# Optimization experiments

Hardware: AMD Instinct MI355X
Metric: run time of the kernel (lower is better)

The kernel has to match this reference:

```python
import jax, jax.numpy as jnp
import numpy as np

P = 128        # num proposals
C_ALL = 19     # instance_classes + 1
C = 18         # instance classes used in the loop
M = 400000     # total (proposal, point) membership entries
N_PTS = 65536  # num points
SCORE_THR = 0.001
MASK_THR = -0.5
NPOINT_THR = 100


def setup_inputs() -> dict:
    key = jax.random.key(0)
    k1, k2, k3, k4, k5 = jax.random.split(key, 5)
    return {
        "cls_scores": jax.random.normal(k1, (P, C_ALL), dtype=jnp.float32),
        "scores": jax.random.normal(k2, (P, C_ALL), dtype=jnp.float32),
        "mask_scores": jax.random.normal(k3, (M, C_ALL), dtype=jnp.float32),
        "prop_ids": jax.random.randint(k4, (M,), 0, P, dtype=jnp.int32),
        "point_ids": jax.random.randint(k5, (M,), 0, N_PTS, dtype=jnp.int32),
        "num_points": N_PTS,
    }


def reference(cls_scores, scores, mask_scores, prop_ids, point_ids, num_points):
    # cls_scores, scores: [P, C+1]; mask_scores: [M, C+1]
    # prop_ids/point_ids: [M] -> membership of point in proposal
    n_prop = cls_scores.shape[0]
    cls_soft = jax.nn.softmax(cls_scores, axis=1)              # [P, C+1]
    # scores_pred_i = clamp(scores[:, i], 0, 1) * cls_soft[:, i], for each class i
    scores_pred = (jnp.clip(scores[:, :C], 0.0, 1.0) * cls_soft[:, :C]).T  # [C, P]

    # per-class mask threshold then scatter 1s into dense [P, N] proposal masks
    mask_keep = (mask_scores[:, :C] > MASK_THR).astype(jnp.int32).T        # [C, M]

    def scatter_one_class(m):
        # duplicates resolved with max (matches repeated assignment of 1)
        return jnp.zeros((n_prop, num_points), jnp.int32).at[prop_ids, point_ids].max(m)

    dense = jax.vmap(scatter_one_class)(mask_keep)             # [C, P, N] int32

    pointnum = dense.sum(axis=-1)                              # [C, P]
    keep = (cls_soft[:, :C].T > SCORE_THR) \
        & (scores_pred > -1.0) \
        & (pointnum >= NPOINT_THR)                             # [C, P]

    proposals_pred = dense * keep[..., None].astype(jnp.int32)  # zero invalid rows
    cluster_scores = jnp.where(keep, scores_pred, 0.0)
    semantic_id = jnp.broadcast_to((jnp.arange(C) + 1)[:, None], (C, n_prop))
    return proposals_pred, cluster_scores, keep, semantic_id
```

## Files before the change

kernel.cpp:

```cpp
#include <hip/hip_runtime.h>
#include <stdint.h>

#define NPROP   128
#define C_ALL   19
#define NCLS    18
#define M_TOTAL 400000
#define NPTS    65536
#define CP      (NCLS * NPROP)
#define PTS_PER_CHUNK 8192
#define NCHUNK  8

typedef float f32x4 __attribute__((ext_vector_type(4)));

struct WS {
    float        spred[CP];
    unsigned int keepA[CP];
    unsigned int pointnum[CP];
    unsigned int dense[(size_t)NPROP * NPTS];
};

__global__ void zero_prep_kernel(const float* __restrict__ cls_scores,
                                 const float* __restrict__ scores, WS* ws) {
    const size_t tid = (size_t)blockIdx.x * blockDim.x + threadIdx.x;
    const size_t stride = (size_t)gridDim.x * blockDim.x;
    uint4* d4 = (uint4*)ws->dense;
    const size_t n4 = (size_t)NPROP * NPTS / 4;
    const uint4 z = make_uint4(0u, 0u, 0u, 0u);
    for (size_t j = tid; j < n4; j += stride) d4[j] = z;
    if (tid < CP) ws->pointnum[tid] = 0;
    if (tid < NPROP) {
        const int p = (int)tid;
        float row[C_ALL];
        float mx = -3.4e38f;
        #pragma unroll
        for (int i = 0; i < C_ALL; ++i) {
            row[i] = cls_scores[p * C_ALL + i];
            mx = fmaxf(mx, row[i]);
        }
        float s = 0.0f;
        #pragma unroll
        for (int i = 0; i < C_ALL; ++i) {
            row[i] = __expf(row[i] - mx);
            s += row[i];
        }
        const float inv = 1.0f / s;
        #pragma unroll
        for (int c = 0; c < NCLS; ++c) {
            const float soft = row[c] * inv;
            float sc = scores[p * C_ALL + c];
            sc = fminf(fmaxf(sc, 0.0f), 1.0f);
            const float sp = sc * soft;
            ws->spred[c * NPROP + p] = sp;
            ws->keepA[c * NPROP + p] = (soft > 0.001f && sp > -1.0f) ? 1u : 0u;
        }
    }
}

__global__ void scatter_kernel(const float* __restrict__ mask_scores,
                               const int* __restrict__ prop_ids,
                               const int* __restrict__ point_ids,
                               WS* ws) {
    int m = blockIdx.x * blockDim.x + threadIdx.x;
    if (m >= M_TOTAL) return;
    const float* r = mask_scores + (size_t)m * C_ALL;
    unsigned int bits = 0;
    #pragma unroll
    for (int c = 0; c < NCLS; ++c)
        bits |= (unsigned int)(r[c] > -0.5f) << c;
    const size_t addr = ((size_t)prop_ids[m] << 16) | (unsigned int)point_ids[m];
    atomicOr(&ws->dense[addr], bits);
}

__global__ __launch_bounds__(256) void count_kernel(WS* ws) {
    __shared__ unsigned int cnt[NCLS];
    const int p = blockIdx.x;
    const int quarter = blockIdx.y;
    const int t = threadIdx.x;
    if (t < NCLS) cnt[t] = 0;
    __syncthreads();
    const uint4* base4 = (const uint4*)(ws->dense + ((size_t)p << 16) +
                                        quarter * (NPTS / 4));
    unsigned int local[NCLS];
    #pragma unroll
    for (int c = 0; c < NCLS; ++c) local[c] = 0;
    #pragma unroll
    for (int j = 0; j < (NPTS / 16) / 256; ++j) {
        const uint4 w = base4[j * 256 + t];
        #pragma unroll
        for (int c = 0; c < NCLS; ++c)
            local[c] += ((w.x >> c) & 1u) + ((w.y >> c) & 1u) +
                        ((w.z >> c) & 1u) + ((w.w >> c) & 1u);
    }
    #pragma unroll
    for (int c = 0; c < NCLS; ++c) {
        unsigned int v = local[c];
        #pragma unroll
        for (int off = 32; off; off >>= 1) v += __shfl_down(v, off, 64);
        if ((t & 63) == 0) atomicAdd(&cnt[c], v);
    }
    __syncthreads();
    if (t < NCLS) atomicAdd(&ws->pointnum[t * NPROP + p], cnt[t]);
}

__global__ __launch_bounds__(256) void write_kernel(const WS* __restrict__ ws,
                                                    float* __restrict__ out) {
    __shared__ unsigned int lds[PTS_PER_CHUNK];
    __shared__ float sk[NCLS];
    const int chunk = blockIdx.x;
    const int p     = blockIdx.y;
    const int t     = threadIdx.x;

    const uint4* src4 = (const uint4*)(ws->dense + ((size_t)p << 16) +
                                       chunk * PTS_PER_CHUNK);
    uint4* lds4 = (uint4*)lds;
    #pragma unroll
    for (int j = 0; j < (PTS_PER_CHUNK / 4) / 256; ++j)
        lds4[j * 256 + t] = src4[j * 256 + t];

    if (t < NCLS) {
        const int cp = t * NPROP + p;
        const bool k = (ws->keepA[cp] != 0u) && (ws->pointnum[cp] >= 100u);
        sk[t] = k ? 1.0f : 0.0f;
        if (chunk == 0) {
            float* outCS = out + (size_t)CP * NPTS;
            float* outK  = outCS + CP;
            float* outS  = outK  + CP;
            outCS[cp] = k ? ws->spred[cp] : 0.0f;
            outK[cp]  = k ? 1.0f : 0.0f;
            outS[cp]  = (float)(t + 1);
        }
    }
    __syncthreads();

    #pragma unroll 1
    for (int c = 0; c < NCLS; ++c) {
        const float kf = sk[c];
        f32x4* dst = (f32x4*)(out + (((size_t)(c * NPROP + p)) << 16)) +
                     chunk * (PTS_PER_CHUNK / 4);
        #pragma unroll
        for (int j = 0; j < (PTS_PER_CHUNK / 4) / 256; ++j) {
            const int idx = j * 256 + t;
            const uint4 w = lds4[idx];
            f32x4 v;
            v.x = ((w.x >> c) & 1u) ? kf : 0.0f;
            v.y = ((w.y >> c) & 1u) ? kf : 0.0f;
            v.z = ((w.z >> c) & 1u) ? kf : 0.0f;
            v.w = ((w.w >> c) & 1u) ? kf : 0.0f;
            __builtin_nontemporal_store(v, &dst[idx]);
        }
    }
}

extern "C" void kernel_launch(void* const* d_in, const int* in_sizes, int n_in,
                              void* d_out, int out_size, void* d_ws, size_t ws_size,
                              hipStream_t stream) {
    const float* cls_scores  = (const float*)d_in[0];
    const float* scores      = (const float*)d_in[1];
    const float* mask_scores = (const float*)d_in[2];
    const int*   prop_ids    = (const int*)d_in[3];
    const int*   point_ids   = (const int*)d_in[4];

    WS* ws = (WS*)d_ws;
    float* out = (float*)d_out;

    zero_prep_kernel<<<2048, 256, 0, stream>>>(cls_scores, scores, ws);
    const int blocksM = (M_TOTAL + 255) / 256;
    scatter_kernel<<<blocksM, 256, 0, stream>>>(mask_scores, prop_ids, point_ids, ws);
    count_kernel<<<dim3(NPROP, 4), 256, 0, stream>>>(ws);
    write_kernel<<<dim3(NCHUNK, NPROP), 256, 0, stream>>>(ws, out);
}
```

Baseline: 177.9 us.

## Write one (class, proposal) output row per block, reading dense bits from global

Measured after the change: 171.9 us. 1.03x faster.

```diff
diff --git a/kernel.cpp b/kernel.cpp
--- a/kernel.cpp
+++ b/kernel.cpp
@@ -7,8 +7,6 @@
 #define M_TOTAL 400000
 #define NPTS    65536
 #define CP      (NCLS * NPROP)
-#define PTS_PER_CHUNK 8192
-#define NCHUNK  8
 
 typedef float f32x4 __attribute__((ext_vector_type(4)));
 
@@ -104,50 +102,35 @@
 
 __global__ __launch_bounds__(256) void write_kernel(const WS* __restrict__ ws,
                                                     float* __restrict__ out) {
-    __shared__ unsigned int lds[PTS_PER_CHUNK];
-    __shared__ float sk[NCLS];
-    const int chunk = blockIdx.x;
-    const int p     = blockIdx.y;
-    const int t     = threadIdx.x;
+    const int cp = blockIdx.x;
+    const int c  = cp / NPROP;
+    const int p  = cp - c * NPROP;
+    const int t  = threadIdx.x;
 
-    const uint4* src4 = (const uint4*)(ws->dense + ((size_t)p << 16) +
-                                       chunk * PTS_PER_CHUNK);
-    uint4* lds4 = (uint4*)lds;
-    #pragma unroll
-    for (int j = 0; j < (PTS_PER_CHUNK / 4) / 256; ++j)
-        lds4[j * 256 + t] = src4[j * 256 + t];
+    const bool keep = (ws->keepA[cp] != 0u) && (ws->pointnum[cp] >= 100u);
+    const float kf = keep ? 1.0f : 0.0f;
 
-    if (t < NCLS) {
-        const int cp = t * NPROP + p;
-        const bool k = (ws->keepA[cp] != 0u) && (ws->pointnum[cp] >= 100u);
-        sk[t] = k ? 1.0f : 0.0f;
-        if (chunk == 0) {
-            float* outCS = out + (size_t)CP * NPTS;
-            float* outK  = outCS + CP;
-            float* outS  = outK  + CP;
-            outCS[cp] = k ? ws->spred[cp] : 0.0f;
-            outK[cp]  = k ? 1.0f : 0.0f;
-            outS[cp]  = (float)(t + 1);
-        }
+    if (t == 0) {
+        float* outCS = out + (size_t)CP * NPTS;
+        float* outK  = outCS + CP;
+        float* outS  = outK  + CP;
+        outCS[cp] = keep ? ws->spred[cp] : 0.0f;
+        outK[cp]  = kf;
+        outS[cp]  = (float)(c + 1);
     }
-    __syncthreads();
 
-    #pragma unroll 1
-    for (int c = 0; c < NCLS; ++c) {
-        const float kf = sk[c];
-        f32x4* dst = (f32x4*)(out + (((size_t)(c * NPROP + p)) << 16)) +
-                     chunk * (PTS_PER_CHUNK / 4);
-        #pragma unroll
-        for (int j = 0; j < (PTS_PER_CHUNK / 4) / 256; ++j) {
-            const int idx = j * 256 + t;
-            const uint4 w = lds4[idx];
-            f32x4 v;
-            v.x = ((w.x >> c) & 1u) ? kf : 0.0f;
-            v.y = ((w.y >> c) & 1u) ? kf : 0.0f;
-            v.z = ((w.z >> c) & 1u) ? kf : 0.0f;
-            v.w = ((w.w >> c) & 1u) ? kf : 0.0f;
-            __builtin_nontemporal_store(v, &dst[idx]);
-        }
+    const uint4* src4 = (const uint4*)(ws->dense + ((size_t)p << 16));
+    f32x4* dst = (f32x4*)(out + ((size_t)cp << 16));
+    #pragma unroll 4
+    for (int j = 0; j < (NPTS / 4) / 256; ++j) {
+        const int idx = j * 256 + t;
+        const uint4 w = src4[idx];
+        f32x4 v;
+        v.x = ((w.x >> c) & 1u) ? kf : 0.0f;
+        v.y = ((w.y >> c) & 1u) ? kf : 0.0f;
+        v.z = ((w.z >> c) & 1u) ? kf : 0.0f;
+        v.w = ((w.w >> c) & 1u) ? kf : 0.0f;
+        dst[idx] = v;
     }
 }
 
@@ -167,5 +150,5 @@
     const int blocksM = (M_TOTAL + 255) / 256;
     scatter_kernel<<<blocksM, 256, 0, stream>>>(mask_scores, prop_ids, point_ids, ws);
     count_kernel<<<dim3(NPROP, 4), 256, 0, stream>>>(ws);
-    write_kernel<<<dim3(NCHUNK, NPROP), 256, 0, stream>>>(ws, out);
+    write_kernel<<<CP, 256, 0, stream>>>(ws, out);
 }
```
